# Kernel tuning notes

Hardware: AMD Instinct MI355X
Metric: run time of the kernel (lower is better)

## Reference

```python
import jax, jax.numpy as jnp
import numpy as np

NUM_CHANNELS = 256
NUM_HEADS = 8
HEAD_DIM = NUM_CHANNELS // NUM_HEADS


def setup_inputs() -> dict:
    key = jax.random.key(0)
    k1, k2, k3, k4, k5 = jax.random.split(key, 5)
    C = NUM_CHANNELS
    s = 1.0 / np.sqrt(C)
    image = jax.random.normal(k1, (8, C, 32, 32), dtype=jnp.float32)
    # kqv_projection: Linear(C, 3C); mix_heads: Linear(C, C). Stored as [in, out].
    w_kqv = jax.random.uniform(k2, (C, 3 * C), minval=-s, maxval=s, dtype=jnp.float32)
    b_kqv = jax.random.uniform(k3, (3 * C,), minval=-s, maxval=s, dtype=jnp.float32)
    w_mix = jax.random.uniform(k4, (C, C), minval=-s, maxval=s, dtype=jnp.float32)
    b_mix = jax.random.uniform(k5, (C,), minval=-s, maxval=s, dtype=jnp.float32)
    return {"image": image, "w_kqv": w_kqv, "b_kqv": b_kqv, "w_mix": w_mix, "b_mix": b_mix}


def _masked_attention(seq, w_kqv, b_kqv, w_mix, b_mix):
    # seq: [N, T, C]
    N, T, C = seq.shape
    H, D = NUM_HEADS, HEAD_DIM
    projected = seq @ w_kqv + b_kqv            # [N, T, 3C]
    k, q, v = jnp.split(projected, 3, axis=-1)  # order: keys, queries, values
    # split heads -> [N, H, T, D]
    k = k.reshape(N, T, H, D).transpose(0, 2, 1, 3)
    q = q.reshape(N, T, H, D).transpose(0, 2, 1, 3)
    v = v.reshape(N, T, H, D).transpose(0, 2, 1, 3)
    logits = jnp.einsum('nhtd,nhsd->nhts', q, k) / jnp.sqrt(jnp.float32(D))
    causal = jnp.tril(jnp.ones((T, T), dtype=bool))
    logits = jnp.where(causal, logits, -jnp.inf)
    weights = jax.nn.softmax(logits, axis=-1)
    out = jnp.einsum('nhts,nhsd->nhtd', weights, v)  # [N, H, T, D]
    out = out.transpose(0, 2, 1, 3).reshape(N, T, C)  # combine heads
    return out @ w_mix + b_mix


def reference(image, w_kqv, b_kqv, w_mix, b_mix):
    N, C, Hh, Ww = image.shape
    seq = image.transpose(0, 2, 3, 1).reshape(N, Hh * Ww, C)
    attn = _masked_attention(seq, w_kqv, b_kqv, w_mix, b_mix)
    attn = attn.reshape(N, Hh, Ww, C).transpose(0, 3, 1, 2)
    return attn + image
```

## Files before the change

kernel.cpp:

```cpp
#include <hip/hip_runtime.h>
#include <math.h>

constexpr int NB  = 8;
constexpr int C   = 256;
constexpr int T   = 1024;
constexpr int NH  = 8;
constexpr int HD  = 32;
constexpr int C3  = 768;

typedef __attribute__((ext_vector_type(8))) short bf16x8;
typedef __attribute__((ext_vector_type(4))) float f32x4;

__device__ inline short f2bf(float f) {
    unsigned u = __float_as_uint(f);
    u += 0x7FFF + ((u >> 16) & 1);
    return (short)(u >> 16);
}

__global__ __launch_bounds__(256) void xpose_bf16(const float* __restrict__ image,
                                                  const float* __restrict__ wkqv,
                                                  const float* __restrict__ wmix,
                                                  short* __restrict__ seqb,
                                                  short* __restrict__ wkqvT,
                                                  short* __restrict__ wmixT) {
    __shared__ float Ld[32][33];
    const int bid = blockIdx.x;
    const float* src; short* dst; int srcStride;
    if (bid < 2048) {
        int nb = bid >> 8, rem = bid & 255, cb = rem >> 5, tb = rem & 31;
        src = image + ((size_t)nb * C + cb * 32) * T + tb * 32;
        dst = seqb + ((size_t)nb * T + tb * 32) * C + cb * 32;
        srcStride = T;
    } else if (bid < 2240) {
        int id = bid - 2048, jb = id >> 3, cb = id & 7;
        src = wkqv + (size_t)(cb * 32) * C3 + jb * 32;
        dst = wkqvT + (size_t)(jb * 32) * C + cb * 32;
        srcStride = C3;
    } else {
        int id = bid - 2240, jb = id >> 3, cb = id & 7;
        src = wmix + (size_t)(cb * 32) * C + jb * 32;
        dst = wmixT + (size_t)(jb * 32) * C + cb * 32;
        srcStride = C;
    }
    const int r = threadIdx.x >> 3, c4 = (threadIdx.x & 7) * 4;
    float4 v = *(const float4*)&src[(size_t)r * srcStride + c4];
    Ld[r][c4 + 0] = v.x; Ld[r][c4 + 1] = v.y; Ld[r][c4 + 2] = v.z; Ld[r][c4 + 3] = v.w;
    __syncthreads();
    short4 o = { f2bf(Ld[c4 + 0][r]), f2bf(Ld[c4 + 1][r]),
                 f2bf(Ld[c4 + 2][r]), f2bf(Ld[c4 + 3][r]) };
    *(short4*)&dst[(size_t)r * C + c4] = o;
}

__global__ __launch_bounds__(256) void kqv_mfma(const short* __restrict__ seqb,
                                                const short* __restrict__ wkqvT,
                                                const float* __restrict__ bkqv,
                                                short* __restrict__ Kb,
                                                short* __restrict__ Qb,
                                                short* __restrict__ Vb) {
    __shared__ __align__(16) short As[128][40];
    __shared__ __align__(16) short Bs[128][40];
    const int tid = threadIdx.x;
    const int n0 = blockIdx.x * 128;
    const int m0 = blockIdx.y * 128;
    const int nb = m0 >> 10, t0 = m0 & 1023;
    const int wv = tid >> 6, lane = tid & 63;
    const int m = lane & 15, quad = lane >> 4;
    const int wr = (wv >> 1) * 64, wc = (wv & 1) * 64;

    f32x4 acc[4][4];
    const f32x4 z = {0.f, 0.f, 0.f, 0.f};
    #pragma unroll
    for (int i = 0; i < 4; ++i)
        #pragma unroll
        for (int j = 0; j < 4; ++j) acc[i][j] = z;

    for (int k0 = 0; k0 < C; k0 += 32) {
        #pragma unroll
        for (int u = 0; u < 2; ++u) {
            int idx = tid + u * 256;
            int r = idx >> 2, c8 = (idx & 3) * 8;
            *(bf16x8*)&As[r][c8] = *(const bf16x8*)&seqb[(size_t)(m0 + r) * C + k0 + c8];
            *(bf16x8*)&Bs[r][c8] = *(const bf16x8*)&wkqvT[(size_t)(n0 + r) * C + k0 + c8];
        }
        __syncthreads();
        bf16x8 a[4], b[4];
        #pragma unroll
        for (int i = 0; i < 4; ++i) a[i] = *(const bf16x8*)&As[wr + 16 * i + m][8 * quad];
        #pragma unroll
        for (int j = 0; j < 4; ++j) b[j] = *(const bf16x8*)&Bs[wc + 16 * j + m][8 * quad];
        #pragma unroll
        for (int i = 0; i < 4; ++i)
            #pragma unroll
            for (int j = 0; j < 4; ++j)
                acc[i][j] = __builtin_amdgcn_mfma_f32_16x16x32_bf16(a[i], b[j], acc[i][j], 0, 0, 0);
        __syncthreads();
    }

    #pragma unroll
    for (int j = 0; j < 4; ++j) {
        int jj = n0 + wc + 16 * j + m;
        int chunk = jj >> 8, hh = (jj >> 5) & 7, d = jj & 31;
        short* dst = (chunk == 0) ? Kb : (chunk == 1) ? Qb : Vb;
        float bias = bkqv[jj];
        float mulv = (chunk == 1) ? 0.17677669529663687f : 1.0f;
        size_t base = (size_t)(nb * NH + hh) * T * HD + d;
        #pragma unroll
        for (int i = 0; i < 4; ++i) {
            int t = t0 + wr + 16 * i + 4 * quad;
            #pragma unroll
            for (int r = 0; r < 4; ++r)
                dst[base + (size_t)(t + r) * HD] = f2bf((acc[i][j][r] + bias) * mulv);
        }
    }
}

__global__ __launch_bounds__(256) void attn_mfma(const short* __restrict__ Kb,
                                                 const short* __restrict__ Qb,
                                                 const short* __restrict__ Vb,
                                                 short* __restrict__ attnb) {
    const int qt = 15 - blockIdx.x;
    const int h  = blockIdx.y;
    const int nb = blockIdx.z;
    const int tid  = threadIdx.x;
    const int wv   = tid >> 6;
    const int lane = tid & 63;
    const int m    = lane & 15;
    const int quad = lane >> 4;

    __shared__ __align__(16) short Qs[64][40];
    __shared__ __align__(16) short Ks[64][40];
    __shared__ __align__(16) short Vt[32][72];
    __shared__ __align__(16) short Ps[64][72];

    const int q0 = qt * 64;
    const size_t hb = (size_t)(nb * NH + h) * T * HD;
    const short* Kp = Kb + hb;
    const short* Qp = Qb + hb;
    const short* Vp = Vb + hb;
    const int sr = tid >> 2, sc8 = (tid & 3) * 8;
    const f32x4 z = {0.f, 0.f, 0.f, 0.f};

    bf16x8 qreg = *(const bf16x8*)&Qp[(size_t)(q0 + sr) * HD + sc8];
    bf16x8 kreg = *(const bf16x8*)&Kp[(size_t)sr * HD + sc8];
    bf16x8 vreg = *(const bf16x8*)&Vp[(size_t)sr * HD + sc8];

    f32x4 O0 = z, O1 = z;
    float lpart[4] = {0.f, 0.f, 0.f, 0.f};

    auto stage = [&](bool withQ) {
        __syncthreads();
        if (withQ) *(bf16x8*)&Qs[sr][sc8] = qreg;
        *(bf16x8*)&Ks[sr][sc8] = kreg;
        #pragma unroll
        for (int i2 = 0; i2 < 8; ++i2) Vt[sc8 + i2][sr] = vreg[i2];
        __syncthreads();
    };

    auto compute = [&](bool last) {
        bf16x8 aq = *(const bf16x8*)&Qs[16 * wv + m][8 * quad];
        f32x4 S[4];
        #pragma unroll
        for (int j = 0; j < 4; ++j) {
            bf16x8 bk = *(const bf16x8*)&Ks[16 * j + m][8 * quad];
            S[j] = __builtin_amdgcn_mfma_f32_16x16x32_bf16(aq, bk, z, 0, 0, 0);
        }
        const int qrow_base = 16 * wv + 4 * quad;
        #pragma unroll
        for (int j = 0; j < 4; ++j)
            #pragma unroll
            for (int r = 0; r < 4; ++r) {
                float e = __expf(S[j][r]);
                if (last && (16 * j + m) > (qrow_base + r)) e = 0.f;
                lpart[r] += e;
                Ps[qrow_base + r][16 * j + m] = f2bf(e);
            }
        #pragma unroll
        for (int kc = 0; kc < 2; ++kc) {
            bf16x8 ap = *(const bf16x8*)&Ps[16 * wv + m][32 * kc + 8 * quad];
            bf16x8 b0 = *(const bf16x8*)&Vt[m][32 * kc + 8 * quad];
            bf16x8 b1 = *(const bf16x8*)&Vt[16 + m][32 * kc + 8 * quad];
            O0 = __builtin_amdgcn_mfma_f32_16x16x32_bf16(ap, b0, O0, 0, 0, 0);
            O1 = __builtin_amdgcn_mfma_f32_16x16x32_bf16(ap, b1, O1, 0, 0, 0);
        }
    };

    for (int st = 0; st < qt; ++st) {
        stage(st == 0);
        kreg = *(const bf16x8*)&Kp[(size_t)((st + 1) * 64 + sr) * HD + sc8];
        vreg = *(const bf16x8*)&Vp[(size_t)((st + 1) * 64 + sr) * HD + sc8];
        compute(false);
    }
    stage(qt == 0);
    compute(true);

    #pragma unroll
    for (int r = 0; r < 4; ++r) {
        float l = lpart[r];
        l += __shfl_xor(l, 1);
        l += __shfl_xor(l, 2);
        l += __shfl_xor(l, 4);
        l += __shfl_xor(l, 8);
        float inv = 1.f / l;
        int row = q0 + 16 * wv + 4 * quad + r;
        short* op = attnb + ((size_t)(nb * T + row)) * C + h * HD;
        op[m]      = f2bf(O0[r] * inv);
        op[16 + m] = f2bf(O1[r] * inv);
    }
}

__global__ __launch_bounds__(256) void mix_mfma(const short* __restrict__ attnb,
                                                const short* __restrict__ wmixT,
                                                const float* __restrict__ bmix,
                                                const float* __restrict__ image,
                                                float* __restrict__ out) {
    __shared__ __align__(16) short As[128][40];
    __shared__ __align__(16) short Bs[64][40];
    const int tid = threadIdx.x;
    const int n0 = blockIdx.x * 64;
    const int m0 = blockIdx.y * 128;
    const int nb = m0 >> 10, t0 = m0 & 1023;
    const int wv = tid >> 6, lane = tid & 63;
    const int m = lane & 15, quad = lane >> 4;

    f32x4 acc[2][4];
    const f32x4 z = {0.f, 0.f, 0.f, 0.f};
    #pragma unroll
    for (int i = 0; i < 2; ++i)
        #pragma unroll
        for (int j = 0; j < 4; ++j) acc[i][j] = z;

    for (int k0 = 0; k0 < C; k0 += 32) {
        #pragma unroll
        for (int u = 0; u < 2; ++u) {
            int idx = tid + u * 256;
            int r = idx >> 2, c8 = (idx & 3) * 8;
            *(bf16x8*)&As[r][c8] = *(const bf16x8*)&attnb[(size_t)(m0 + r) * C + k0 + c8];
        }
        {
            int r = tid >> 2, c8 = (tid & 3) * 8;
            *(bf16x8*)&Bs[r][c8] = *(const bf16x8*)&wmixT[(size_t)(n0 + r) * C + k0 + c8];
        }
        __syncthreads();
        bf16x8 a[2], b[4];
        #pragma unroll
        for (int i = 0; i < 2; ++i) a[i] = *(const bf16x8*)&As[32 * wv + 16 * i + m][8 * quad];
        #pragma unroll
        for (int j = 0; j < 4; ++j) b[j] = *(const bf16x8*)&Bs[16 * j + m][8 * quad];
        #pragma unroll
        for (int i = 0; i < 2; ++i)
            #pragma unroll
            for (int j = 0; j < 4; ++j)
                acc[i][j] = __builtin_amdgcn_mfma_f32_16x16x32_bf16(a[i], b[j], acc[i][j], 0, 0, 0);
        __syncthreads();
    }

    #pragma unroll
    for (int j = 0; j < 4; ++j) {
        int c = n0 + 16 * j + m;
        float bias = bmix[c];
        #pragma unroll
        for (int i = 0; i < 2; ++i) {
            int t = t0 + 32 * wv + 16 * i + 4 * quad;
            size_t o = (size_t)(nb * C + c) * T + t;
            float4 img = *(const float4*)&image[o];
            float4 res = { acc[i][j][0] + bias + img.x,
                           acc[i][j][1] + bias + img.y,
                           acc[i][j][2] + bias + img.z,
                           acc[i][j][3] + bias + img.w };
            *(float4*)&out[o] = res;
        }
    }
}

extern "C" void kernel_launch(void* const* d_in, const int* in_sizes, int n_in,
                              void* d_out, int out_size, void* d_ws, size_t ws_size,
                              hipStream_t stream) {
    const float* image = (const float*)d_in[0];
    const float* w_kqv = (const float*)d_in[1];
    const float* b_kqv = (const float*)d_in[2];
    const float* w_mix = (const float*)d_in[3];
    const float* b_mix = (const float*)d_in[4];
    float* out = (float*)d_out;

    short* seqb  = (short*)d_ws;
    short* wkqvT = seqb  + (size_t)NB * T * C;
    short* wmixT = wkqvT + (size_t)C3 * C;
    short* Kb    = wmixT + (size_t)C * C;
    short* Qb    = Kb    + (size_t)NB * NH * T * HD;
    short* Vb    = Qb    + (size_t)NB * NH * T * HD;
    short* attnb = Vb    + (size_t)NB * NH * T * HD;

    xpose_bf16<<<2304, 256, 0, stream>>>(image, w_kqv, w_mix, seqb, wkqvT, wmixT);
    kqv_mfma<<<dim3(C3 / 128, NB * T / 128), 256, 0, stream>>>(seqb, wkqvT, b_kqv, Kb, Qb, Vb);
    attn_mfma<<<dim3(16, NH, NB), 256, 0, stream>>>(Kb, Qb, Vb, attnb);
    mix_mfma<<<dim3(C / 64, NB * T / 128), 256, 0, stream>>>(attnb, wmixT, b_mix, image, out);
}
```

Before: 121.8 us.

## Retile GEMMs to 64x64 with register prefetch, double-buffer attention with 128-row query tiles

The two projection GEMMs drop to 64x64 tiles with one wave per 16 rows, and they prefetch the next K slice into registers so global loads overlap MFMA work. The attention kernel now handles 128 query rows per block and double-buffers the K/V tiles in shared memory, which removes one barrier per step. It also folds log2(e) into the Q scale so it can use exp2, and it truncates P to bf16 instead of rounding it. This trades more GEMM blocks with less reuse and fewer attention blocks for better latency hiding, with a small precision change.

```diff
diff --git a/kernel.cpp b/kernel.cpp
--- a/kernel.cpp
+++ b/kernel.cpp
@@ -8,6 +8,8 @@
 constexpr int HD  = 32;
 constexpr int C3  = 768;
 
+constexpr float QSCALE = 0.25503489422229562f;
+
 typedef __attribute__((ext_vector_type(8))) short bf16x8;
 typedef __attribute__((ext_vector_type(4))) float f32x4;
 
@@ -15,6 +17,9 @@
     unsigned u = __float_as_uint(f);
     u += 0x7FFF + ((u >> 16) & 1);
     return (short)(u >> 16);
+}
+__device__ inline short f2bf_trunc(float f) {
+    return (short)(__float_as_uint(f) >> 16);
 }
 
 __global__ __launch_bounds__(256) void xpose_bf16(const float* __restrict__ image,
@@ -57,60 +62,54 @@
                                                 short* __restrict__ Kb,
                                                 short* __restrict__ Qb,
                                                 short* __restrict__ Vb) {
-    __shared__ __align__(16) short As[128][40];
-    __shared__ __align__(16) short Bs[128][40];
+    __shared__ __align__(16) short As[64][40];
+    __shared__ __align__(16) short Bs[64][40];
     const int tid = threadIdx.x;
-    const int n0 = blockIdx.x * 128;
-    const int m0 = blockIdx.y * 128;
+    const int n0 = blockIdx.x * 64;
+    const int m0 = blockIdx.y * 64;
     const int nb = m0 >> 10, t0 = m0 & 1023;
     const int wv = tid >> 6, lane = tid & 63;
     const int m = lane & 15, quad = lane >> 4;
-    const int wr = (wv >> 1) * 64, wc = (wv & 1) * 64;
-
-    f32x4 acc[4][4];
+    const int sr = tid >> 2, sc8 = (tid & 3) * 8;
+
+    f32x4 acc[4];
     const f32x4 z = {0.f, 0.f, 0.f, 0.f};
     #pragma unroll
-    for (int i = 0; i < 4; ++i)
-        #pragma unroll
-        for (int j = 0; j < 4; ++j) acc[i][j] = z;
+    for (int j = 0; j < 4; ++j) acc[j] = z;
+
+    bf16x8 areg = *(const bf16x8*)&seqb[(size_t)(m0 + sr) * C + sc8];
+    bf16x8 breg = *(const bf16x8*)&wkqvT[(size_t)(n0 + sr) * C + sc8];
 
     for (int k0 = 0; k0 < C; k0 += 32) {
-        #pragma unroll
-        for (int u = 0; u < 2; ++u) {
-            int idx = tid + u * 256;
-            int r = idx >> 2, c8 = (idx & 3) * 8;
-            *(bf16x8*)&As[r][c8] = *(const bf16x8*)&seqb[(size_t)(m0 + r) * C + k0 + c8];
-            *(bf16x8*)&Bs[r][c8] = *(const bf16x8*)&wkqvT[(size_t)(n0 + r) * C + k0 + c8];
-        }
-        __syncthreads();
-        bf16x8 a[4], b[4];
-        #pragma unroll
-        for (int i = 0; i < 4; ++i) a[i] = *(const bf16x8*)&As[wr + 16 * i + m][8 * quad];
-        #pragma unroll
-        for (int j = 0; j < 4; ++j) b[j] = *(const bf16x8*)&Bs[wc + 16 * j + m][8 * quad];
-        #pragma unroll
-        for (int i = 0; i < 4; ++i)
-            #pragma unroll
-            for (int j = 0; j < 4; ++j)
-                acc[i][j] = __builtin_amdgcn_mfma_f32_16x16x32_bf16(a[i], b[j], acc[i][j], 0, 0, 0);
-        __syncthreads();
+        __syncthreads();
+        *(bf16x8*)&As[sr][sc8] = areg;
+        *(bf16x8*)&Bs[sr][sc8] = breg;
+        if (k0 + 32 < C) {
+            areg = *(const bf16x8*)&seqb[(size_t)(m0 + sr) * C + k0 + 32 + sc8];
+            breg = *(const bf16x8*)&wkqvT[(size_t)(n0 + sr) * C + k0 + 32 + sc8];
+        }
+        __syncthreads();
+        bf16x8 a = *(const bf16x8*)&As[16 * wv + m][8 * quad];
+        bf16x8 b[4];
+        #pragma unroll
+        for (int j = 0; j < 4; ++j) b[j] = *(const bf16x8*)&Bs[16 * j + m][8 * quad];
+        #pragma unroll
+        for (int j = 0; j < 4; ++j)
+            acc[j] = __builtin_amdgcn_mfma_f32_16x16x32_bf16(a, b[j], acc[j], 0, 0, 0);
     }
 
     #pragma unroll
     for (int j = 0; j < 4; ++j) {
-        int jj = n0 + wc + 16 * j + m;
+        int jj = n0 + 16 * j + m;
         int chunk = jj >> 8, hh = (jj >> 5) & 7, d = jj & 31;
         short* dst = (chunk == 0) ? Kb : (chunk == 1) ? Qb : Vb;
         float bias = bkqv[jj];
-        float mulv = (chunk == 1) ? 0.17677669529663687f : 1.0f;
+        float mul = (chunk == 1) ? QSCALE : 1.0f;
         size_t base = (size_t)(nb * NH + hh) * T * HD + d;
-        #pragma unroll
-        for (int i = 0; i < 4; ++i) {
-            int t = t0 + wr + 16 * i + 4 * quad;
-            #pragma unroll
-            for (int r = 0; r < 4; ++r)
-                dst[base + (size_t)(t + r) * HD] = f2bf((acc[i][j][r] + bias) * mulv);
-        }
+        int t = t0 + 16 * wv + 4 * quad;
+        #pragma unroll
+        for (int r = 0; r < 4; ++r)
+            dst[base + (size_t)(t + r) * HD] = f2bf((acc[j][r] + bias) * mul);
     }
 }
 
@@ -118,7 +117,7 @@
                                                  const short* __restrict__ Qb,
                                                  const short* __restrict__ Vb,
                                                  short* __restrict__ attnb) {
-    const int qt = 15 - blockIdx.x;
+    const int qb = 7 - blockIdx.x;
     const int h  = blockIdx.y;
     const int nb = blockIdx.z;
     const int tid  = threadIdx.x;
@@ -127,12 +126,13 @@
     const int m    = lane & 15;
     const int quad = lane >> 4;
 
-    __shared__ __align__(16) short Qs[64][40];
-    __shared__ __align__(16) short Ks[64][40];
-    __shared__ __align__(16) short Vt[32][72];
-    __shared__ __align__(16) short Ps[64][72];
-
-    const int q0 = qt * 64;
+    __shared__ __align__(16) short Qs[128][40];
+    __shared__ __align__(16) short Ks[2][64][40];
+    __shared__ __align__(16) short Vt[2][32][72];
+    __shared__ __align__(16) short Ps[128][72];
+
+    const int q0  = qb * 128;
+    const int nst = 2 * qb + 2;
     const size_t hb = (size_t)(nb * NH + h) * T * HD;
     const short* Kp = Kb + hb;
     const short* Qp = Qb + hb;
@@ -140,72 +140,92 @@
     const int sr = tid >> 2, sc8 = (tid & 3) * 8;
     const f32x4 z = {0.f, 0.f, 0.f, 0.f};
 
-    bf16x8 qreg = *(const bf16x8*)&Qp[(size_t)(q0 + sr) * HD + sc8];
+    bf16x8 qr0  = *(const bf16x8*)&Qp[(size_t)(q0 + sr) * HD + sc8];
+    bf16x8 qr1  = *(const bf16x8*)&Qp[(size_t)(q0 + 64 + sr) * HD + sc8];
     bf16x8 kreg = *(const bf16x8*)&Kp[(size_t)sr * HD + sc8];
     bf16x8 vreg = *(const bf16x8*)&Vp[(size_t)sr * HD + sc8];
-
-    f32x4 O0 = z, O1 = z;
-    float lpart[4] = {0.f, 0.f, 0.f, 0.f};
-
-    auto stage = [&](bool withQ) {
-        __syncthreads();
-        if (withQ) *(bf16x8*)&Qs[sr][sc8] = qreg;
-        *(bf16x8*)&Ks[sr][sc8] = kreg;
-        #pragma unroll
-        for (int i2 = 0; i2 < 8; ++i2) Vt[sc8 + i2][sr] = vreg[i2];
-        __syncthreads();
-    };
-
-    auto compute = [&](bool last) {
-        bf16x8 aq = *(const bf16x8*)&Qs[16 * wv + m][8 * quad];
-        f32x4 S[4];
-        #pragma unroll
-        for (int j = 0; j < 4; ++j) {
-            bf16x8 bk = *(const bf16x8*)&Ks[16 * j + m][8 * quad];
-            S[j] = __builtin_amdgcn_mfma_f32_16x16x32_bf16(aq, bk, z, 0, 0, 0);
-        }
-        const int qrow_base = 16 * wv + 4 * quad;
-        #pragma unroll
-        for (int j = 0; j < 4; ++j)
+    *(bf16x8*)&Qs[sr][sc8]      = qr0;
+    *(bf16x8*)&Qs[64 + sr][sc8] = qr1;
+    *(bf16x8*)&Ks[0][sr][sc8]   = kreg;
+    #pragma unroll
+    for (int i2 = 0; i2 < 8; ++i2) Vt[0][sc8 + i2][sr] = vreg[i2];
+
+    f32x4 O[2][2] = {{z, z}, {z, z}};
+    float lp[2][4] = {};
+
+    for (int st = 0; st < nst; ++st) {
+        const int p = st & 1;
+        __syncthreads();
+        if (st + 1 < nst) {
+            kreg = *(const bf16x8*)&Kp[(size_t)((st + 1) * 64 + sr) * HD + sc8];
+            vreg = *(const bf16x8*)&Vp[(size_t)((st + 1) * 64 + sr) * HD + sc8];
+        }
+
+        bf16x8 bk[4];
+        #pragma unroll
+        for (int j = 0; j < 4; ++j) bk[j] = *(const bf16x8*)&Ks[p][16 * j + m][8 * quad];
+        f32x4 S[2][4];
+        #pragma unroll
+        for (int i = 0; i < 2; ++i) {
+            bf16x8 aq = *(const bf16x8*)&Qs[32 * wv + 16 * i + m][8 * quad];
             #pragma unroll
-            for (int r = 0; r < 4; ++r) {
-                float e = __expf(S[j][r]);
-                if (last && (16 * j + m) > (qrow_base + r)) e = 0.f;
-                lpart[r] += e;
-                Ps[qrow_base + r][16 * j + m] = f2bf(e);
+            for (int j = 0; j < 4; ++j)
+                S[i][j] = __builtin_amdgcn_mfma_f32_16x16x32_bf16(aq, bk[j], z, 0, 0, 0);
+        }
+
+        const bool msk = (st >= 2 * qb);
+        const int s0 = st * 64;
+        #pragma unroll
+        for (int i = 0; i < 2; ++i) {
+            const int qr_base = q0 + 32 * wv + 16 * i + 4 * quad;
+            #pragma unroll
+            for (int j = 0; j < 4; ++j) {
+                const int sc = s0 + 16 * j + m;
+                #pragma unroll
+                for (int r = 0; r < 4; ++r) {
+                    float e = __builtin_amdgcn_exp2f(S[i][j][r]);
+                    if (msk && sc > qr_base + r) e = 0.f;
+                    lp[i][r] += e;
+                    Ps[32 * wv + 16 * i + 4 * quad + r][16 * j + m] = f2bf_trunc(e);
+                }
             }
+        }
+
         #pragma unroll
         for (int kc = 0; kc < 2; ++kc) {
-            bf16x8 ap = *(const bf16x8*)&Ps[16 * wv + m][32 * kc + 8 * quad];
-            bf16x8 b0 = *(const bf16x8*)&Vt[m][32 * kc + 8 * quad];
-            bf16x8 b1 = *(const bf16x8*)&Vt[16 + m][32 * kc + 8 * quad];
-            O0 = __builtin_amdgcn_mfma_f32_16x16x32_bf16(ap, b0, O0, 0, 0, 0);
-            O1 = __builtin_amdgcn_mfma_f32_16x16x32_bf16(ap, b1, O1, 0, 0, 0);
-        }
-    };
-
-    for (int st = 0; st < qt; ++st) {
-        stage(st == 0);
-        kreg = *(const bf16x8*)&Kp[(size_t)((st + 1) * 64 + sr) * HD + sc8];
-        vreg = *(const bf16x8*)&Vp[(size_t)((st + 1) * 64 + sr) * HD + sc8];
-        compute(false);
-    }
-    stage(qt == 0);
-    compute(true);
-
-    #pragma unroll
-    for (int r = 0; r < 4; ++r) {
-        float l = lpart[r];
-        l += __shfl_xor(l, 1);
-        l += __shfl_xor(l, 2);
-        l += __shfl_xor(l, 4);
-        l += __shfl_xor(l, 8);
-        float inv = 1.f / l;
-        int row = q0 + 16 * wv + 4 * quad + r;
-        short* op = attnb + ((size_t)(nb * T + row)) * C + h * HD;
-        op[m]      = f2bf(O0[r] * inv);
-        op[16 + m] = f2bf(O1[r] * inv);
-    }
+            bf16x8 ap0 = *(const bf16x8*)&Ps[32 * wv + m][32 * kc + 8 * quad];
+            bf16x8 ap1 = *(const bf16x8*)&Ps[32 * wv + 16 + m][32 * kc + 8 * quad];
+            bf16x8 b0  = *(const bf16x8*)&Vt[p][m][32 * kc + 8 * quad];
+            bf16x8 b1  = *(const bf16x8*)&Vt[p][16 + m][32 * kc + 8 * quad];
+            O[0][0] = __builtin_amdgcn_mfma_f32_16x16x32_bf16(ap0, b0, O[0][0], 0, 0, 0);
+            O[0][1] = __builtin_amdgcn_mfma_f32_16x16x32_bf16(ap0, b1, O[0][1], 0, 0, 0);
+            O[1][0] = __builtin_amdgcn_mfma_f32_16x16x32_bf16(ap1, b0, O[1][0], 0, 0, 0);
+            O[1][1] = __builtin_amdgcn_mfma_f32_16x16x32_bf16(ap1, b1, O[1][1], 0, 0, 0);
+        }
+
+        if (st + 1 < nst) {
+            const int pn = p ^ 1;
+            *(bf16x8*)&Ks[pn][sr][sc8] = kreg;
+            #pragma unroll
+            for (int i2 = 0; i2 < 8; ++i2) Vt[pn][sc8 + i2][sr] = vreg[i2];
+        }
+    }
+
+    #pragma unroll
+    for (int i = 0; i < 2; ++i)
+        #pragma unroll
+        for (int r = 0; r < 4; ++r) {
+            float l = lp[i][r];
+            l += __shfl_xor(l, 1);
+            l += __shfl_xor(l, 2);
+            l += __shfl_xor(l, 4);
+            l += __shfl_xor(l, 8);
+            float inv = 1.f / l;
+            int row = q0 + 32 * wv + 16 * i + 4 * quad + r;
+            short* op = attnb + ((size_t)(nb * T + row)) * C + h * HD;
+            op[m]      = f2bf(O[i][0][r] * inv);
+            op[16 + m] = f2bf(O[i][1][r] * inv);
+        }
 }
 
 __global__ __launch_bounds__(256) void mix_mfma(const short* __restrict__ attnb,
@@ -213,62 +233,54 @@
                                                 const float* __restrict__ bmix,
                                                 const float* __restrict__ image,
                                                 float* __restrict__ out) {
-    __shared__ __align__(16) short As[128][40];
+    __shared__ __align__(16) short As[64][40];
     __shared__ __align__(16) short Bs[64][40];
     const int tid = threadIdx.x;
     const int n0 = blockIdx.x * 64;
-    const int m0 = blockIdx.y * 128;
+    const int m0 = blockIdx.y * 64;
     const int nb = m0 >> 10, t0 = m0 & 1023;
     const int wv = tid >> 6, lane = tid & 63;
     const int m = lane & 15, quad = lane >> 4;
-
-    f32x4 acc[2][4];
+    const int sr = tid >> 2, sc8 = (tid & 3) * 8;
+
+    f32x4 acc[4];
     const f32x4 z = {0.f, 0.f, 0.f, 0.f};
     #pragma unroll
-    for (int i = 0; i < 2; ++i)
-        #pragma unroll
-        for (int j = 0; j < 4; ++j) acc[i][j] = z;
+    for (int j = 0; j < 4; ++j) acc[j] = z;
+
+    bf16x8 areg = *(const bf16x8*)&attnb[(size_t)(m0 + sr) * C + sc8];
+    bf16x8 breg = *(const bf16x8*)&wmixT[(size_t)(n0 + sr) * C + sc8];
 
     for (int k0 = 0; k0 < C; k0 += 32) {
-        #pragma unroll
-        for (int u = 0; u < 2; ++u) {
-            int idx = tid + u * 256;
-            int r = idx >> 2, c8 = (idx & 3) * 8;
-            *(bf16x8*)&As[r][c8] = *(const bf16x8*)&attnb[(size_t)(m0 + r) * C + k0 + c8];
-        }
-        {
-            int r = tid >> 2, c8 = (tid & 3) * 8;
-            *(bf16x8*)&Bs[r][c8] = *(const bf16x8*)&wmixT[(size_t)(n0 + r) * C + k0 + c8];
-        }
-        __syncthreads();
-        bf16x8 a[2], b[4];
-        #pragma unroll
-        for (int i = 0; i < 2; ++i) a[i] = *(const bf16x8*)&As[32 * wv + 16 * i + m][8 * quad];
+        __syncthreads();
+        *(bf16x8*)&As[sr][sc8] = areg;
+        *(bf16x8*)&Bs[sr][sc8] = breg;
+        if (k0 + 32 < C) {
+            areg = *(const bf16x8*)&attnb[(size_t)(m0 + sr) * C + k0 + 32 + sc8];
+            breg = *(const bf16x8*)&wmixT[(size_t)(n0 + sr) * C + k0 + 32 + sc8];
+        }
+        __syncthreads();
+        bf16x8 a = *(const bf16x8*)&As[16 * wv + m][8 * quad];
+        bf16x8 b[4];
         #pragma unroll
         for (int j = 0; j < 4; ++j) b[j] = *(const bf16x8*)&Bs[16 * j + m][8 * quad];
         #pragma unroll
-        for (int i = 0; i < 2; ++i)
-            #pragma unroll
-            for (int j = 0; j < 4; ++j)
-                acc[i][j] = __builtin_amdgcn_mfma_f32_16x16x32_bf16(a[i], b[j], acc[i][j], 0, 0, 0);
-        __syncthreads();
-    }
-
+        for (int j = 0; j < 4; ++j)
+            acc[j] = __builtin_amdgcn_mfma_f32_16x16x32_bf16(a, b[j], acc[j], 0, 0, 0);
+    }
+
+    const int tb = t0 + 16 * wv + 4 * quad;
     #pragma unroll
     for (int j = 0; j < 4; ++j) {
         int c = n0 + 16 * j + m;
         float bias = bmix[c];
-        #pragma unroll
-        for (int i = 0; i < 2; ++i) {
-            int t = t0 + 32 * wv + 16 * i + 4 * quad;
-            size_t o = (size_t)(nb * C + c) * T + t;
-            float4 img = *(const float4*)&image[o];
-            float4 res = { acc[i][j][0] + bias + img.x,
-                           acc[i][j][1] + bias + img.y,
-                           acc[i][j][2] + bias + img.z,
-                           acc[i][j][3] + bias + img.w };
-            *(float4*)&out[o] = res;
-        }
+        size_t o = (size_t)(nb * C + c) * T + tb;
+        float4 img = *(const float4*)&image[o];
+        float4 res = { acc[j][0] + bias + img.x,
+                       acc[j][1] + bias + img.y,
+                       acc[j][2] + bias + img.z,
+                       acc[j][3] + bias + img.w };
+        *(float4*)&out[o] = res;
     }
 }
 
@@ -291,7 +303,7 @@
     short* attnb = Vb    + (size_t)NB * NH * T * HD;
 
     xpose_bf16<<<2304, 256, 0, stream>>>(image, w_kqv, w_mix, seqb, wkqvT, wmixT);
-    kqv_mfma<<<dim3(C3 / 128, NB * T / 128), 256, 0, stream>>>(seqb, wkqvT, b_kqv, Kb, Qb, Vb);
-    attn_mfma<<<dim3(16, NH, NB), 256, 0, stream>>>(Kb, Qb, Vb, attnb);
-    mix_mfma<<<dim3(C / 64, NB * T / 128), 256, 0, stream>>>(attnb, wmixT, b_mix, image, out);
-}
+    kqv_mfma<<<dim3(C3 / 64, NB * T / 64), 256, 0, stream>>>(seqb, wkqvT, b_kqv, Kb, Qb, Vb);
+    attn_mfma<<<dim3(8, NH, NB), 256, 0, stream>>>(Kb, Qb, Vb, attnb);
+    mix_mfma<<<dim3(C / 64, NB * T / 64), 256, 0, stream>>>(attnb, wmixT, b_mix, image, out);
+}
```

Result: faster. 115.8 us (-4.9%).
